# Optimization experiments

Measured on AMD Instinct MI355X. Metric: run time of the kernel, lower is better.

The kernel has to match this reference:

```python
import jax, jax.numpy as jnp
import numpy as np
from jax import lax

GAMMA = 1.0       # SoftDTW gamma (init default)
MAX_DIST = 10000.0  # clamp in SoftDTW.forward
# bandwidth=None -> 0 -> Sakoe-Chiba pruning disabled (condition 0 < bandwidth never holds)


def _softdtw(D, gamma):
    """Soft-DTW DP via anti-diagonal wavefront scan. D: (B, N, M) -> (B,)."""
    B, N, M = D.shape
    R = jnp.full((B, N + 2, M + 2), jnp.inf, D.dtype).at[:, 0, 0].set(0.0)
    i_vec = jnp.arange(1, N + 1)  # row indices of interior cells

    def step(R, p):
        # cells on anti-diagonal p satisfy i + j == p + 2
        j_vec = p + 2 - i_vec
        valid = (j_vec >= 1) & (j_vec <= M)
        jc = jnp.clip(j_vec, 1, M)
        r0 = R[:, i_vec - 1, jc - 1]  # (B, N) diag
        r1 = R[:, i_vec - 1, jc]      # up
        r2 = R[:, i_vec, jc - 1]      # left
        neg = jnp.stack([r0, r1, r2], axis=0) * (-1.0 / gamma)  # (3, B, N)
        # invalid lanes: keep finite to avoid NaNs (result discarded by where)
        neg = jnp.where(valid[None, None, :], neg, 0.0)
        softmin = -gamma * jax.scipy.special.logsumexp(neg, axis=0)  # (B, N)
        new = D[:, i_vec - 1, jc - 1] + softmin
        R = R.at[:, i_vec, jc].set(jnp.where(valid[None, :], new, R[:, i_vec, jc]))
        return R, None

    R, _ = lax.scan(step, R, jnp.arange(N + M - 1))
    return R[:, N, M]


def setup_inputs() -> dict:
    key = jax.random.key(0)
    kx, ky = jax.random.split(key)
    X = jax.random.normal(kx, (16, 512, 64), dtype=jnp.float32)
    Y = jax.random.normal(ky, (16, 512, 64), dtype=jnp.float32)
    return {"X": X, "Y": Y}


def reference(X, Y):
    # squared Euclidean pairwise distance per timestep (faithful expand form)
    D = jnp.sum((X[:, :, None, :] - Y[:, None, :, :]) ** 2, axis=-1)  # (B, N, M)
    D = jnp.minimum(D, MAX_DIST)
    return _softdtw(D, GAMMA)
```

## Files before the change

### kernel.cpp

```cpp
#include <hip/hip_runtime.h>

#define BIGF 1e30f
#define LOG2E 1.4426950408889634f
#define LN2F 0.6931471805599453f

constexpr int NB = 16;
constexpr int NN = 512;
constexpr int MM = 512;
constexpr int KD = 64;
constexpr int WAVES = 8;
constexpr int CSPAN = 32;
constexpr int NSPANS = 32;
constexpr int SPW = 18;
constexpr int TPH = 3 * (WAVES - 1) + SPW;
constexpr int DIAGELEMS = NN * MM;

constexpr int BBSTRIDE = 672;
constexpr int BUFD_FLOATS = WAVES * 2 * CSPAN * 64;
constexpr int BBUF_FLOATS = WAVES * BBSTRIDE;
constexpr int SMEM_BYTES = (BUFD_FLOATS + BBUF_FLOATS) * 4;

__device__ __forceinline__ int Bclosed(int s) {
  return (s <= 511) ? (s * (s + 1)) / 2
                    : DIAGELEMS - ((1023 - s) * (1024 - s)) / 2 - (s - 511);
}

__global__ __launch_bounds__(256) void pairdist_kernel(
    const float* __restrict__ X, const float* __restrict__ Y,
    float* __restrict__ Dsk) {
  const int b = blockIdx.z;
  const int i0 = blockIdx.y * 64;
  const int j0 = blockIdx.x * 64;

  __shared__ float Xs[64][65];
  __shared__ float Ys[64][65];
  __shared__ float Ds[64][66];

  const float* Xb = X + ((size_t)b * NN + i0) * KD;
  const float* Yb = Y + ((size_t)b * MM + j0) * KD;
  for (int k = threadIdx.x; k < 64 * KD; k += 256) {
    Xs[k >> 6][k & 63] = Xb[k];
    Ys[k >> 6][k & 63] = Yb[k];
  }
  __syncthreads();

  const int tx = threadIdx.x & 15;
  const int ty = threadIdx.x >> 4;
  const int r0 = ty * 4, c0 = tx * 4;

  float acc[4][4];
#pragma unroll
  for (int a = 0; a < 4; ++a)
#pragma unroll
    for (int e = 0; e < 4; ++e) acc[a][e] = 0.0f;

  for (int d = 0; d < KD; ++d) {
    float xv[4], yv[4];
#pragma unroll
    for (int q = 0; q < 4; ++q) xv[q] = Xs[r0 + q][d];
#pragma unroll
    for (int q = 0; q < 4; ++q) yv[q] = Ys[c0 + q][d];
#pragma unroll
    for (int a = 0; a < 4; ++a)
#pragma unroll
      for (int e = 0; e < 4; ++e) {
        float df = xv[a] - yv[e];
        acc[a][e] = fmaf(df, df, acc[a][e]);
      }
  }

#pragma unroll
  for (int a = 0; a < 4; ++a)
#pragma unroll
    for (int e = 0; e < 4; ++e)
      Ds[r0 + a][c0 + e] = fminf(acc[a][e], 10000.0f) * LOG2E;
  __syncthreads();

  const int wv = threadIdx.x >> 6;
  const int ln = threadIdx.x & 63;
  float* Db = Dsk + (size_t)b * DIAGELEMS;
  for (int sl = wv; sl < 127; sl += 4) {
    const int istart = sl > 63 ? sl - 63 : 0;
    const int iend = sl < 63 ? sl : 63;
    if (ln <= iend - istart) {
      const int ig = i0 + istart + ln;
      Db[Bclosed(i0 + j0 + sl) + ig] = Ds[istart + ln][sl - istart - ln];
    }
  }
}

__device__ __forceinline__ float dpp_shr1_old(float oldv, float v) {
  return __int_as_float(__builtin_amdgcn_update_dpp(
      __float_as_int(oldv), __float_as_int(v), 0x138 , 0xf, 0xf,
      false));
}
__device__ __forceinline__ float dpp_shl1(float v) {
  return __int_as_float(__builtin_amdgcn_update_dpp(
      __float_as_int(v), __float_as_int(v), 0x130 , 0xf, 0xf,
      false));
}

__device__ __forceinline__ float fexp2(float x) {
  x = fmaxf(x, -126.0f);
  return __int_as_float((int)fmaf(x, 8388608.0f, 1.064975338e9f));
}
__device__ __forceinline__ float flog2(float y) {
  return fmaf((float)__float_as_int(y), 1.1920929e-7f, -126.9549534f);
}

__device__ __forceinline__ void dma_span(const float* __restrict__ Dskb,
                                         float* bufD, int blk, int q,
                                         int lane) {
  float* dst0 = bufD + (blk * 2 + (q & 1)) * (CSPAN * 64);
  const int rbase = 64 * blk + (lane & 15) * 4;
  const int sub = lane >> 4;
#pragma unroll
  for (int u = 0; u < 8; ++u) {
    int s = 32 * q + 4 * u + sub;
    s = s > 1022 ? 1022 : s;
    int e = Bclosed(s) + rbase;
    e = e > DIAGELEMS - 4 ? DIAGELEMS - 4 : e;
    __builtin_amdgcn_global_load_lds(
        (const __attribute__((address_space(1))) void*)(Dskb + e),
        (__attribute__((address_space(3))) void*)(dst0 + u * 256), 16, 0, 0);
  }
}

#define SOFTMIN_STEP(K)                                                     \
  {                                                                         \
    const float up1 = dpp_shr1_old(B, ra);                                  \
    B = dpp_shl1(B);                                                        \
    const float m = fminf(fminf(up1, up2), ra);                             \
    const float md = __builtin_amdgcn_fmed3f(up1, up2, ra);                 \
    const float mx = fmaxf(fmaxf(up1, up2), ra);                            \
    const float ssum = (fexp2(m - md) + fexp2(m - mx)) + 1.0f;              \
    n = (dv[K] + m) - flog2(ssum);                                          \
    up2 = up1;                                                              \
  }

extern __shared__ float smem[];
__global__ __launch_bounds__(512) void softdtw_kernel(
    const float* __restrict__ Dsk, float* __restrict__ out) {
  const int b = blockIdx.x;
  const int t = threadIdx.x;
  const int wu = __builtin_amdgcn_readfirstlane(t >> 6);
  const int lane = t & 63;
  const int blk = ((wu & 3) << 1) | (wu >> 2);

  float* bufD = smem;
  float* bbuf = smem + BUFD_FLOATS;

  for (int k = t; k < BBUF_FLOATS; k += 512) bbuf[k] = BIGF;
  __syncthreads();

  const float* __restrict__ Dskb = Dsk + (size_t)b * DIAGELEMS;

  dma_span(Dskb, bufD, blk, 2 * blk, lane);

  const int r = 64 * blk + lane;
  float ra = BIGF;
  float up2 = (blk == 0 && lane == 0) ? 0.0f : BIGF;

  for (int S = 0; S < TPH; ++S) {
    const int cc = S - 3 * blk;
    if (cc >= 0 && cc < SPW) {
      const int c = cc + 2 * blk;
      if (cc + 1 < SPW) {
        dma_span(Dskb, bufD, blk, c + 1, lane);
        asm volatile("s_waitcnt vmcnt(8)" ::: "memory");
      } else {
        asm volatile("s_waitcnt vmcnt(0)" ::: "memory");
      }

      float B = BIGF;
      if (blk) B = bbuf[blk * BBSTRIDE + 62 + 32 * cc + 1 + lane];

      const float* myD = bufD + (blk * 2 + (c & 1)) * (CSPAN * 64);
      const __attribute__((address_space(3))) float* mp =
          (const __attribute__((address_space(3))) float*)(myD + lane);
      unsigned maddr = (unsigned)(size_t)mp;

      float dv[CSPAN];
      asm volatile(
          "ds_read_b32 %0, %32 offset:0\n\t"
          "ds_read_b32 %1, %32 offset:256\n\t"
          "ds_read_b32 %2, %32 offset:512\n\t"
          "ds_read_b32 %3, %32 offset:768\n\t"
          "ds_read_b32 %4, %32 offset:1024\n\t"
          "ds_read_b32 %5, %32 offset:1280\n\t"
          "ds_read_b32 %6, %32 offset:1536\n\t"
          "ds_read_b32 %7, %32 offset:1792\n\t"
          "ds_read_b32 %8, %32 offset:2048\n\t"
          "ds_read_b32 %9, %32 offset:2304\n\t"
          "ds_read_b32 %10, %32 offset:2560\n\t"
          "ds_read_b32 %11, %32 offset:2816\n\t"
          "ds_read_b32 %12, %32 offset:3072\n\t"
          "ds_read_b32 %13, %32 offset:3328\n\t"
          "ds_read_b32 %14, %32 offset:3584\n\t"
          "ds_read_b32 %15, %32 offset:3840\n\t"
          "ds_read_b32 %16, %32 offset:4096\n\t"
          "ds_read_b32 %17, %32 offset:4352\n\t"
          "ds_read_b32 %18, %32 offset:4608\n\t"
          "ds_read_b32 %19, %32 offset:4864\n\t"
          "ds_read_b32 %20, %32 offset:5120\n\t"
          "ds_read_b32 %21, %32 offset:5376\n\t"
          "ds_read_b32 %22, %32 offset:5632\n\t"
          "ds_read_b32 %23, %32 offset:5888\n\t"
          "ds_read_b32 %24, %32 offset:6144\n\t"
          "ds_read_b32 %25, %32 offset:6400\n\t"
          "ds_read_b32 %26, %32 offset:6656\n\t"
          "ds_read_b32 %27, %32 offset:6912\n\t"
          "ds_read_b32 %28, %32 offset:7168\n\t"
          "ds_read_b32 %29, %32 offset:7424\n\t"
          "ds_read_b32 %30, %32 offset:7680\n\t"
          "ds_read_b32 %31, %32 offset:7936\n\t"
          "s_waitcnt lgkmcnt(0)"
          : "=&v"(dv[0]), "=&v"(dv[1]), "=&v"(dv[2]), "=&v"(dv[3]),
            "=&v"(dv[4]), "=&v"(dv[5]), "=&v"(dv[6]), "=&v"(dv[7]),
            "=&v"(dv[8]), "=&v"(dv[9]), "=&v"(dv[10]), "=&v"(dv[11]),
            "=&v"(dv[12]), "=&v"(dv[13]), "=&v"(dv[14]), "=&v"(dv[15]),
            "=&v"(dv[16]), "=&v"(dv[17]), "=&v"(dv[18]), "=&v"(dv[19]),
            "=&v"(dv[20]), "=&v"(dv[21]), "=&v"(dv[22]), "=&v"(dv[23]),
            "=&v"(dv[24]), "=&v"(dv[25]), "=&v"(dv[26]), "=&v"(dv[27]),
            "=&v"(dv[28]), "=&v"(dv[29]), "=&v"(dv[30]), "=&v"(dv[31])
          : "v"(maddr)
          : "memory");

      float* pubp =
          bbuf + ((blk + 1) & 7) * BBSTRIDE + (62 + 32 * c - r + 1);

      float n;
      if (cc >= 2 && cc <= 15) {
#pragma unroll
        for (int k = 0; k < CSPAN; ++k) {
          SOFTMIN_STEP(k);
          ra = n;
          pubp[k] = ra;
        }
      } else {
        const int jv0 = 32 * c - r + 1;
#pragma unroll
        for (int k = 0; k < CSPAN; ++k) {
          SOFTMIN_STEP(k);
          const bool a0 = (unsigned)(jv0 + k - 1) < (unsigned)MM;
          ra = a0 ? n : ra;
          pubp[k] = ra;
        }
      }
    }
    asm volatile("s_waitcnt lgkmcnt(0)" ::: "memory");
    __builtin_amdgcn_s_barrier();
  }

  if (blk == WAVES - 1 && lane == 63) out[b] = ra * LN2F;
}

extern "C" void kernel_launch(void* const* d_in, const int* in_sizes, int n_in,
                              void* d_out, int out_size, void* d_ws,
                              size_t ws_size, hipStream_t stream) {
  const float* X = (const float*)d_in[0];
  const float* Y = (const float*)d_in[1];
  float* out = (float*)d_out;
  float* Dsk = (float*)d_ws;

  const size_t needed = (size_t)NB * DIAGELEMS * sizeof(float);
  if (ws_size < needed) return;

  hipFuncSetAttribute((const void*)softdtw_kernel,
                      hipFuncAttributeMaxDynamicSharedMemorySize, SMEM_BYTES);

  pairdist_kernel<<<dim3(MM / 64, NN / 64, NB), 256, 0, stream>>>(X, Y, Dsk);
  softdtw_kernel<<<NB, 512, SMEM_BYTES, stream>>>(Dsk, out);
}
```

Baseline: 135.4 us.

## Widen wavefront spans to 64 columns and shorten inter-wave skew

Each wave now processes 64 anti-diagonal steps per phase instead of 32, with a wave-to-wave skew of 2 spans rather than 3. This cuts the number of barrier-separated phases and shrinks the pipeline fill/drain overhead. LDS double-buffering of D is dropped: the single buffer is read into registers first, then the next span's DMA is issued and awaited with vmcnt(0) at the start of the next phase. That exposes less prefetch slack and doubles per-phase register use for the D values.

```diff
diff --git a/kernel.cpp b/kernel.cpp
--- a/kernel.cpp
+++ b/kernel.cpp
@@ -9,14 +9,15 @@
 constexpr int MM = 512;
 constexpr int KD = 64;
 constexpr int WAVES = 8;
-constexpr int CSPAN = 32;
-constexpr int NSPANS = 32;
-constexpr int SPW = 18;
-constexpr int TPH = 3 * (WAVES - 1) + SPW;
+constexpr int CSPAN = 64;
+constexpr int NSPANS = 16;
+constexpr int SPW = 9;
+constexpr int OFF = 2;
+constexpr int TPH = OFF * (WAVES - 1) + SPW;
 constexpr int DIAGELEMS = NN * MM;
 
-constexpr int BBSTRIDE = 672;
-constexpr int BUFD_FLOATS = WAVES * 2 * CSPAN * 64;
+constexpr int BBSTRIDE = 640;
+constexpr int BUFD_FLOATS = WAVES * CSPAN * 64;
 constexpr int BBUF_FLOATS = WAVES * BBSTRIDE;
 constexpr int SMEM_BYTES = (BUFD_FLOATS + BBUF_FLOATS) * 4;
 
@@ -111,12 +112,12 @@
 __device__ __forceinline__ void dma_span(const float* __restrict__ Dskb,
                                          float* bufD, int blk, int q,
                                          int lane) {
-  float* dst0 = bufD + (blk * 2 + (q & 1)) * (CSPAN * 64);
+  float* dst0 = bufD + blk * (CSPAN * 64);
   const int rbase = 64 * blk + (lane & 15) * 4;
   const int sub = lane >> 4;
 #pragma unroll
-  for (int u = 0; u < 8; ++u) {
-    int s = 32 * q + 4 * u + sub;
+  for (int u = 0; u < 16; ++u) {
+    int s = 64 * q + 4 * u + sub;
     s = s > 1022 ? 1022 : s;
     int e = Bclosed(s) + rbase;
     e = e > DIAGELEMS - 4 ? DIAGELEMS - 4 : e;
@@ -126,7 +127,52 @@
   }
 }
 
-#define SOFTMIN_STEP(K)                                                     \
+#define DS_READ32(DV, ADDR, TAIL)                                           \
+  asm volatile(                                                             \
+      "ds_read_b32 %0, %32 offset:0\n\t"                                    \
+      "ds_read_b32 %1, %32 offset:256\n\t"                                  \
+      "ds_read_b32 %2, %32 offset:512\n\t"                                  \
+      "ds_read_b32 %3, %32 offset:768\n\t"                                  \
+      "ds_read_b32 %4, %32 offset:1024\n\t"                                 \
+      "ds_read_b32 %5, %32 offset:1280\n\t"                                 \
+      "ds_read_b32 %6, %32 offset:1536\n\t"                                 \
+      "ds_read_b32 %7, %32 offset:1792\n\t"                                 \
+      "ds_read_b32 %8, %32 offset:2048\n\t"                                 \
+      "ds_read_b32 %9, %32 offset:2304\n\t"                                 \
+      "ds_read_b32 %10, %32 offset:2560\n\t"                                \
+      "ds_read_b32 %11, %32 offset:2816\n\t"                                \
+      "ds_read_b32 %12, %32 offset:3072\n\t"                                \
+      "ds_read_b32 %13, %32 offset:3328\n\t"                                \
+      "ds_read_b32 %14, %32 offset:3584\n\t"                                \
+      "ds_read_b32 %15, %32 offset:3840\n\t"                                \
+      "ds_read_b32 %16, %32 offset:4096\n\t"                                \
+      "ds_read_b32 %17, %32 offset:4352\n\t"                                \
+      "ds_read_b32 %18, %32 offset:4608\n\t"                                \
+      "ds_read_b32 %19, %32 offset:4864\n\t"                                \
+      "ds_read_b32 %20, %32 offset:5120\n\t"                                \
+      "ds_read_b32 %21, %32 offset:5376\n\t"                                \
+      "ds_read_b32 %22, %32 offset:5632\n\t"                                \
+      "ds_read_b32 %23, %32 offset:5888\n\t"                                \
+      "ds_read_b32 %24, %32 offset:6144\n\t"                                \
+      "ds_read_b32 %25, %32 offset:6400\n\t"                                \
+      "ds_read_b32 %26, %32 offset:6656\n\t"                                \
+      "ds_read_b32 %27, %32 offset:6912\n\t"                                \
+      "ds_read_b32 %28, %32 offset:7168\n\t"                                \
+      "ds_read_b32 %29, %32 offset:7424\n\t"                                \
+      "ds_read_b32 %30, %32 offset:7680\n\t"                                \
+      "ds_read_b32 %31, %32 offset:7936\n\t" TAIL                           \
+      : "=&v"(DV[0]), "=&v"(DV[1]), "=&v"(DV[2]), "=&v"(DV[3]),             \
+        "=&v"(DV[4]), "=&v"(DV[5]), "=&v"(DV[6]), "=&v"(DV[7]),             \
+        "=&v"(DV[8]), "=&v"(DV[9]), "=&v"(DV[10]), "=&v"(DV[11]),           \
+        "=&v"(DV[12]), "=&v"(DV[13]), "=&v"(DV[14]), "=&v"(DV[15]),         \
+        "=&v"(DV[16]), "=&v"(DV[17]), "=&v"(DV[18]), "=&v"(DV[19]),         \
+        "=&v"(DV[20]), "=&v"(DV[21]), "=&v"(DV[22]), "=&v"(DV[23]),         \
+        "=&v"(DV[24]), "=&v"(DV[25]), "=&v"(DV[26]), "=&v"(DV[27]),         \
+        "=&v"(DV[28]), "=&v"(DV[29]), "=&v"(DV[30]), "=&v"(DV[31])          \
+      : "v"(ADDR)                                                           \
+      : "memory")
+
+#define SOFTMIN_STEP(DVK)                                                   \
   {                                                                         \
     const float up1 = dpp_shr1_old(B, ra);                                  \
     B = dpp_shl1(B);                                                        \
@@ -134,7 +180,7 @@
     const float md = __builtin_amdgcn_fmed3f(up1, up2, ra);                 \
     const float mx = fmaxf(fmaxf(up1, up2), ra);                            \
     const float ssum = (fexp2(m - md) + fexp2(m - mx)) + 1.0f;              \
-    n = (dv[K] + m) - flog2(ssum);                                          \
+    n = ((DVK) + m) - flog2(ssum);                                          \
     up2 = up1;                                                              \
   }
 
@@ -155,93 +201,50 @@
 
   const float* __restrict__ Dskb = Dsk + (size_t)b * DIAGELEMS;
 
-  dma_span(Dskb, bufD, blk, 2 * blk, lane);
+  dma_span(Dskb, bufD, blk, blk, lane);
 
   const int r = 64 * blk + lane;
   float ra = BIGF;
   float up2 = (blk == 0 && lane == 0) ? 0.0f : BIGF;
 
   for (int S = 0; S < TPH; ++S) {
-    const int cc = S - 3 * blk;
+    const int cc = S - OFF * blk;
     if (cc >= 0 && cc < SPW) {
-      const int c = cc + 2 * blk;
-      if (cc + 1 < SPW) {
-        dma_span(Dskb, bufD, blk, c + 1, lane);
-        asm volatile("s_waitcnt vmcnt(8)" ::: "memory");
-      } else {
-        asm volatile("s_waitcnt vmcnt(0)" ::: "memory");
-      }
+      const int c = cc + blk;
+      asm volatile("s_waitcnt vmcnt(0)" ::: "memory");
 
       float B = BIGF;
-      if (blk) B = bbuf[blk * BBSTRIDE + 62 + 32 * cc + 1 + lane];
-
-      const float* myD = bufD + (blk * 2 + (c & 1)) * (CSPAN * 64);
+      if (blk) B = bbuf[blk * BBSTRIDE + 62 + 64 * cc + 1 + lane];
+
+      const float* myD = bufD + blk * (CSPAN * 64);
       const __attribute__((address_space(3))) float* mp =
           (const __attribute__((address_space(3))) float*)(myD + lane);
       unsigned maddr = (unsigned)(size_t)mp;
 
-      float dv[CSPAN];
-      asm volatile(
-          "ds_read_b32 %0, %32 offset:0\n\t"
-          "ds_read_b32 %1, %32 offset:256\n\t"
-          "ds_read_b32 %2, %32 offset:512\n\t"
-          "ds_read_b32 %3, %32 offset:768\n\t"
-          "ds_read_b32 %4, %32 offset:1024\n\t"
-          "ds_read_b32 %5, %32 offset:1280\n\t"
-          "ds_read_b32 %6, %32 offset:1536\n\t"
-          "ds_read_b32 %7, %32 offset:1792\n\t"
-          "ds_read_b32 %8, %32 offset:2048\n\t"
-          "ds_read_b32 %9, %32 offset:2304\n\t"
-          "ds_read_b32 %10, %32 offset:2560\n\t"
-          "ds_read_b32 %11, %32 offset:2816\n\t"
-          "ds_read_b32 %12, %32 offset:3072\n\t"
-          "ds_read_b32 %13, %32 offset:3328\n\t"
-          "ds_read_b32 %14, %32 offset:3584\n\t"
-          "ds_read_b32 %15, %32 offset:3840\n\t"
-          "ds_read_b32 %16, %32 offset:4096\n\t"
-          "ds_read_b32 %17, %32 offset:4352\n\t"
-          "ds_read_b32 %18, %32 offset:4608\n\t"
-          "ds_read_b32 %19, %32 offset:4864\n\t"
-          "ds_read_b32 %20, %32 offset:5120\n\t"
-          "ds_read_b32 %21, %32 offset:5376\n\t"
-          "ds_read_b32 %22, %32 offset:5632\n\t"
-          "ds_read_b32 %23, %32 offset:5888\n\t"
-          "ds_read_b32 %24, %32 offset:6144\n\t"
-          "ds_read_b32 %25, %32 offset:6400\n\t"
-          "ds_read_b32 %26, %32 offset:6656\n\t"
-          "ds_read_b32 %27, %32 offset:6912\n\t"
-          "ds_read_b32 %28, %32 offset:7168\n\t"
-          "ds_read_b32 %29, %32 offset:7424\n\t"
-          "ds_read_b32 %30, %32 offset:7680\n\t"
-          "ds_read_b32 %31, %32 offset:7936\n\t"
-          "s_waitcnt lgkmcnt(0)"
-          : "=&v"(dv[0]), "=&v"(dv[1]), "=&v"(dv[2]), "=&v"(dv[3]),
-            "=&v"(dv[4]), "=&v"(dv[5]), "=&v"(dv[6]), "=&v"(dv[7]),
-            "=&v"(dv[8]), "=&v"(dv[9]), "=&v"(dv[10]), "=&v"(dv[11]),
-            "=&v"(dv[12]), "=&v"(dv[13]), "=&v"(dv[14]), "=&v"(dv[15]),
-            "=&v"(dv[16]), "=&v"(dv[17]), "=&v"(dv[18]), "=&v"(dv[19]),
-            "=&v"(dv[20]), "=&v"(dv[21]), "=&v"(dv[22]), "=&v"(dv[23]),
-            "=&v"(dv[24]), "=&v"(dv[25]), "=&v"(dv[26]), "=&v"(dv[27]),
-            "=&v"(dv[28]), "=&v"(dv[29]), "=&v"(dv[30]), "=&v"(dv[31])
-          : "v"(maddr)
-          : "memory");
+      float dvlo[32], dvhi[32];
+      DS_READ32(dvlo, maddr, "s_nop 0");
+      DS_READ32(dvhi, maddr + 8192, "s_waitcnt lgkmcnt(0)");
+
+      if (cc + 1 < SPW) dma_span(Dskb, bufD, blk, c + 1, lane);
 
       float* pubp =
-          bbuf + ((blk + 1) & 7) * BBSTRIDE + (62 + 32 * c - r + 1);
+          bbuf + ((blk + 1) & 7) * BBSTRIDE + (62 + 64 * c - r + 1);
 
       float n;
-      if (cc >= 2 && cc <= 15) {
+      if (cc >= 1 && cc <= 7) {
 #pragma unroll
         for (int k = 0; k < CSPAN; ++k) {
-          SOFTMIN_STEP(k);
+          const float dval = (k < 32) ? dvlo[k] : dvhi[k - 32];
+          SOFTMIN_STEP(dval);
           ra = n;
           pubp[k] = ra;
         }
       } else {
-        const int jv0 = 32 * c - r + 1;
+        const int jv0 = 64 * c - r + 1;
 #pragma unroll
         for (int k = 0; k < CSPAN; ++k) {
-          SOFTMIN_STEP(k);
+          const float dval = (k < 32) ? dvlo[k] : dvhi[k - 32];
+          SOFTMIN_STEP(dval);
           const bool a0 = (unsigned)(jv0 + k - 1) < (unsigned)MM;
           ra = a0 ? n : ra;
           pubp[k] = ra;
```

Result: slower. 145.5 us (+7.4%).

## Assign two DP rows per lane with four waves instead of eight

Applied to the files above, without the earlier changes.

The soft-DTW wavefront kernel now runs 4 waves per batch, with each lane computing two adjacent rows (128 rows per wave) instead of one row per lane across 8 waves. The intra-lane row pair passes values through registers, cross-lane row hand-off uses readlane plus one DPP shift, and D tiles are read as float2 with ds_read_b64. This cuts the number of wave-to-wave pipeline stages and barrier-synchronised handoffs along the diagonal, and halves per-cell LDS read instructions. In exchange each step has a longer serial dependency chain (two cells per step) and per-wave DMA volume doubles.

```diff
diff --git a/kernel.cpp b/kernel.cpp
--- a/kernel.cpp
+++ b/kernel.cpp
@@ -8,15 +8,16 @@
 constexpr int NN = 512;
 constexpr int MM = 512;
 constexpr int KD = 64;
-constexpr int WAVES = 8;
+constexpr int WAVES = 4;
 constexpr int CSPAN = 32;
 constexpr int NSPANS = 32;
-constexpr int SPW = 18;
-constexpr int TPH = 3 * (WAVES - 1) + SPW;
+constexpr int SPW = 20;
+constexpr int TPH = 5 * (WAVES - 1) + SPW;
 constexpr int DIAGELEMS = NN * MM;
 
-constexpr int BBSTRIDE = 672;
-constexpr int BUFD_FLOATS = WAVES * 2 * CSPAN * 64;
+constexpr int BBPAD = 126;
+constexpr int BBSTRIDE = 768;
+constexpr int BUFD_FLOATS = WAVES * 2 * CSPAN * 128;
 constexpr int BBUF_FLOATS = WAVES * BBSTRIDE;
 constexpr int SMEM_BYTES = (BUFD_FLOATS + BBUF_FLOATS) * 4;
 
@@ -94,11 +95,6 @@
       __float_as_int(oldv), __float_as_int(v), 0x138 , 0xf, 0xf,
       false));
 }
-__device__ __forceinline__ float dpp_shl1(float v) {
-  return __int_as_float(__builtin_amdgcn_update_dpp(
-      __float_as_int(v), __float_as_int(v), 0x130 , 0xf, 0xf,
-      false));
-}
 
 __device__ __forceinline__ float fexp2(float x) {
   x = fmaxf(x, -126.0f);
@@ -109,14 +105,13 @@
 }
 
 __device__ __forceinline__ void dma_span(const float* __restrict__ Dskb,
-                                         float* bufD, int blk, int q,
-                                         int lane) {
-  float* dst0 = bufD + (blk * 2 + (q & 1)) * (CSPAN * 64);
-  const int rbase = 64 * blk + (lane & 15) * 4;
-  const int sub = lane >> 4;
-#pragma unroll
-  for (int u = 0; u < 8; ++u) {
-    int s = 32 * q + 4 * u + sub;
+                                         float* bufD, int w, int q, int lane) {
+  float* dst0 = bufD + (w * 2 + (q & 1)) * (CSPAN * 128);
+  const int rbase = 128 * w + (lane & 31) * 4;
+  const int sub = lane >> 5;
+#pragma unroll
+  for (int u = 0; u < 16; ++u) {
+    int s = 32 * q + 2 * u + sub;
     s = s > 1022 ? 1022 : s;
     int e = Bclosed(s) + rbase;
     e = e > DIAGELEMS - 4 ? DIAGELEMS - 4 : e;
@@ -126,94 +121,102 @@
   }
 }
 
-#define SOFTMIN_STEP(K)                                                     \
+#define CELL(DVAL, A, Bv, C, NOUT)                                          \
   {                                                                         \
-    const float up1 = dpp_shr1_old(B, ra);                                  \
-    B = dpp_shl1(B);                                                        \
-    const float m = fminf(fminf(up1, up2), ra);                             \
-    const float md = __builtin_amdgcn_fmed3f(up1, up2, ra);                 \
-    const float mx = fmaxf(fmaxf(up1, up2), ra);                            \
-    const float ssum = (fexp2(m - md) + fexp2(m - mx)) + 1.0f;              \
-    n = (dv[K] + m) - flog2(ssum);                                          \
-    up2 = up1;                                                              \
-  }
+    const float m_ = fminf(fminf((A), (Bv)), (C));                          \
+    const float md_ = __builtin_amdgcn_fmed3f((A), (Bv), (C));              \
+    const float mx_ = fmaxf(fmaxf((A), (Bv)), (C));                         \
+    const float ss_ = (fexp2(m_ - md_) + fexp2(m_ - mx_)) + 1.0f;           \
+    NOUT = ((DVAL) + m_) - flog2(ss_);                                      \
+  }
+
+#define STEP_CORE(K)                                                        \
+  const float o1 = __int_as_float(                                          \
+      __builtin_amdgcn_readlane(__float_as_int(browA), K));                 \
+  const float up1 = dpp_shr1_old(o1, ra1);                                  \
+  const float up2 = up2c;                                                   \
+  up2c = up1;                                                               \
+  float n0, n1;                                                             \
+  CELL(dv[K].x, up1, up2, ra0, n0);                                         \
+  CELL(dv[K].y, ra0, rb0, ra1, n1);
 
 extern __shared__ float smem[];
-__global__ __launch_bounds__(512) void softdtw_kernel(
+__global__ __launch_bounds__(256) void softdtw_kernel(
     const float* __restrict__ Dsk, float* __restrict__ out) {
   const int b = blockIdx.x;
   const int t = threadIdx.x;
-  const int wu = __builtin_amdgcn_readfirstlane(t >> 6);
+  const int w = __builtin_amdgcn_readfirstlane(t >> 6);
   const int lane = t & 63;
-  const int blk = ((wu & 3) << 1) | (wu >> 2);
 
   float* bufD = smem;
   float* bbuf = smem + BUFD_FLOATS;
 
-  for (int k = t; k < BBUF_FLOATS; k += 512) bbuf[k] = BIGF;
+  for (int k = t; k < BBUF_FLOATS; k += 256) bbuf[k] = BIGF;
   __syncthreads();
 
   const float* __restrict__ Dskb = Dsk + (size_t)b * DIAGELEMS;
 
-  dma_span(Dskb, bufD, blk, 2 * blk, lane);
-
-  const int r = 64 * blk + lane;
-  float ra = BIGF;
-  float up2 = (blk == 0 && lane == 0) ? 0.0f : BIGF;
+  dma_span(Dskb, bufD, w, 4 * w, lane);
+
+  const int r0 = 128 * w + 2 * lane;
+  float ra0 = BIGF, rb0 = BIGF;
+  float ra1 = BIGF;
+  float up2c = (w == 0 && lane == 0) ? 0.0f : BIGF;
 
   for (int S = 0; S < TPH; ++S) {
-    const int cc = S - 3 * blk;
+    const int cc = S - 5 * w;
     if (cc >= 0 && cc < SPW) {
-      const int c = cc + 2 * blk;
+      const int c = cc + 4 * w;
       if (cc + 1 < SPW) {
-        dma_span(Dskb, bufD, blk, c + 1, lane);
-        asm volatile("s_waitcnt vmcnt(8)" ::: "memory");
+        dma_span(Dskb, bufD, w, c + 1, lane);
+        asm volatile("s_waitcnt vmcnt(16)" ::: "memory");
       } else {
         asm volatile("s_waitcnt vmcnt(0)" ::: "memory");
       }
 
-      float B = BIGF;
-      if (blk) B = bbuf[blk * BBSTRIDE + 62 + 32 * cc + 1 + lane];
-
-      const float* myD = bufD + (blk * 2 + (c & 1)) * (CSPAN * 64);
+      int bi = BBPAD + 32 * cc + 1 + lane;
+      bi = bi > BBSTRIDE - 1 ? BBSTRIDE - 1 : bi;
+      const float browA = w ? bbuf[w * BBSTRIDE + bi] : BIGF;
+
+      const float* myD = bufD + (w * 2 + (c & 1)) * (CSPAN * 128);
       const __attribute__((address_space(3))) float* mp =
-          (const __attribute__((address_space(3))) float*)(myD + lane);
+          (const __attribute__((address_space(3))) float*)(myD + 2 * lane);
       unsigned maddr = (unsigned)(size_t)mp;
 
-      float dv[CSPAN];
+      float2 dv[CSPAN];
       asm volatile(
-          "ds_read_b32 %0, %32 offset:0\n\t"
-          "ds_read_b32 %1, %32 offset:256\n\t"
-          "ds_read_b32 %2, %32 offset:512\n\t"
-          "ds_read_b32 %3, %32 offset:768\n\t"
-          "ds_read_b32 %4, %32 offset:1024\n\t"
-          "ds_read_b32 %5, %32 offset:1280\n\t"
-          "ds_read_b32 %6, %32 offset:1536\n\t"
-          "ds_read_b32 %7, %32 offset:1792\n\t"
-          "ds_read_b32 %8, %32 offset:2048\n\t"
-          "ds_read_b32 %9, %32 offset:2304\n\t"
-          "ds_read_b32 %10, %32 offset:2560\n\t"
-          "ds_read_b32 %11, %32 offset:2816\n\t"
-          "ds_read_b32 %12, %32 offset:3072\n\t"
-          "ds_read_b32 %13, %32 offset:3328\n\t"
-          "ds_read_b32 %14, %32 offset:3584\n\t"
-          "ds_read_b32 %15, %32 offset:3840\n\t"
-          "ds_read_b32 %16, %32 offset:4096\n\t"
-          "ds_read_b32 %17, %32 offset:4352\n\t"
-          "ds_read_b32 %18, %32 offset:4608\n\t"
-          "ds_read_b32 %19, %32 offset:4864\n\t"
-          "ds_read_b32 %20, %32 offset:5120\n\t"
-          "ds_read_b32 %21, %32 offset:5376\n\t"
-          "ds_read_b32 %22, %32 offset:5632\n\t"
-          "ds_read_b32 %23, %32 offset:5888\n\t"
-          "ds_read_b32 %24, %32 offset:6144\n\t"
-          "ds_read_b32 %25, %32 offset:6400\n\t"
-          "ds_read_b32 %26, %32 offset:6656\n\t"
-          "ds_read_b32 %27, %32 offset:6912\n\t"
-          "ds_read_b32 %28, %32 offset:7168\n\t"
-          "ds_read_b32 %29, %32 offset:7424\n\t"
-          "ds_read_b32 %30, %32 offset:7680\n\t"
-          "ds_read_b32 %31, %32 offset:7936\n\t"
+          "ds_read_b64 %0, %32 offset:0\n\t"
+          "ds_read_b64 %1, %32 offset:512\n\t"
+          "ds_read_b64 %2, %32 offset:1024\n\t"
+          "ds_read_b64 %3, %32 offset:1536\n\t"
+          "ds_read_b64 %4, %32 offset:2048\n\t"
+          "ds_read_b64 %5, %32 offset:2560\n\t"
+          "ds_read_b64 %6, %32 offset:3072\n\t"
+          "ds_read_b64 %7, %32 offset:3584\n\t"
+          "ds_read_b64 %8, %32 offset:4096\n\t"
+          "ds_read_b64 %9, %32 offset:4608\n\t"
+          "ds_read_b64 %10, %32 offset:5120\n\t"
+          "ds_read_b64 %11, %32 offset:5632\n\t"
+          "ds_read_b64 %12, %32 offset:6144\n\t"
+          "ds_read_b64 %13, %32 offset:6656\n\t"
+          "ds_read_b64 %14, %32 offset:7168\n\t"
+          "ds_read_b64 %15, %32 offset:7680\n\t"
+          "ds_read_b64 %16, %32 offset:8192\n\t"
+          "ds_read_b64 %17, %32 offset:8704\n\t"
+          "ds_read_b64 %18, %32 offset:9216\n\t"
+          "ds_read_b64 %19, %32 offset:9728\n\t"
+          "ds_read_b64 %20, %32 offset:10240\n\t"
+          "ds_read_b64 %21, %32 offset:10752\n\t"
+          "ds_read_b64 %22, %32 offset:11264\n\t"
+          "ds_read_b64 %23, %32 offset:11776\n\t"
+          "ds_read_b64 %24, %32 offset:12288\n\t"
+          "ds_read_b64 %25, %32 offset:12800\n\t"
+          "ds_read_b64 %26, %32 offset:13312\n\t"
+          "ds_read_b64 %27, %32 offset:13824\n\t"
+          "ds_read_b64 %28, %32 offset:14336\n\t"
+          "ds_read_b64 %29, %32 offset:14848\n\t"
+          "ds_read_b64 %30, %32 offset:15360\n\t"
+          "ds_read_b64 %31, %32 offset:15872\n\t"
           "s_waitcnt lgkmcnt(0)"
           : "=&v"(dv[0]), "=&v"(dv[1]), "=&v"(dv[2]), "=&v"(dv[3]),
             "=&v"(dv[4]), "=&v"(dv[5]), "=&v"(dv[6]), "=&v"(dv[7]),
@@ -227,24 +230,28 @@
           : "memory");
 
       float* pubp =
-          bbuf + ((blk + 1) & 7) * BBSTRIDE + (62 + 32 * c - r + 1);
-
-      float n;
-      if (cc >= 2 && cc <= 15) {
+          bbuf + ((w + 1) & 3) * BBSTRIDE + (BBPAD + 32 * cc - 2 * lane);
+
+      if (cc >= 4 && cc <= 15) {
 #pragma unroll
         for (int k = 0; k < CSPAN; ++k) {
-          SOFTMIN_STEP(k);
-          ra = n;
-          pubp[k] = ra;
+          STEP_CORE(k);
+          rb0 = ra0;
+          ra0 = n0;
+          ra1 = n1;
+          pubp[k] = n1;
         }
       } else {
-        const int jv0 = 32 * c - r + 1;
+        const int jv0 = 32 * cc + 1 - 2 * lane;
 #pragma unroll
         for (int k = 0; k < CSPAN; ++k) {
-          SOFTMIN_STEP(k);
+          STEP_CORE(k);
           const bool a0 = (unsigned)(jv0 + k - 1) < (unsigned)MM;
-          ra = a0 ? n : ra;
-          pubp[k] = ra;
+          const bool a1 = (unsigned)(jv0 + k - 2) < (unsigned)MM;
+          rb0 = a0 ? ra0 : rb0;
+          ra0 = a0 ? n0 : ra0;
+          ra1 = a1 ? n1 : ra1;
+          pubp[k] = n1;
         }
       }
     }
@@ -252,7 +259,7 @@
     __builtin_amdgcn_s_barrier();
   }
 
-  if (blk == WAVES - 1 && lane == 63) out[b] = ra * LN2F;
+  if (w == WAVES - 1 && lane == 63) out[b] = ra1 * LN2F;
 }
 
 extern "C" void kernel_launch(void* const* d_in, const int* in_sizes, int n_in,
@@ -270,5 +277,5 @@
                       hipFuncAttributeMaxDynamicSharedMemorySize, SMEM_BYTES);
 
   pairdist_kernel<<<dim3(MM / 64, NN / 64, NB), 256, 0, stream>>>(X, Y, Dsk);
-  softdtw_kernel<<<NB, 512, SMEM_BYTES, stream>>>(Dsk, out);
-}
+  softdtw_kernel<<<NB, 256, SMEM_BYTES, stream>>>(Dsk, out);
+}
```

Result: slower. 152.1 us (+12.3%).
